# Kernel tuning notes

Hardware: AMD Instinct MI355X
Metric: run time of the kernel (lower is better)

Reference implementation:

```python
import jax, jax.numpy as jnp
import numpy as np

D_MODEL = 1024
NUM_HEADS = 16
D_K = D_MODEL // NUM_HEADS


def setup_inputs() -> dict:
    key = jax.random.key(0)
    ks = jax.random.split(key, 16)
    B, S, D = 4, 2048, D_MODEL
    scale = 1.0 / np.sqrt(D)
    inp = {
        'Xs': jax.random.normal(ks[0], (B, S, D), jnp.float32),
        'Xt': jax.random.normal(ks[1], (B, S, D), jnp.float32),
    }
    names = ['qs', 'qt', 'ks', 'kt', 'vs', 'vt']
    for i, n in enumerate(names):
        inp['W_' + n] = jax.random.normal(ks[2 + 2 * i], (D, D), jnp.float32) * scale
        inp['b_' + n] = jax.random.normal(ks[3 + 2 * i], (D,), jnp.float32) * 0.01
    inp['attn_bias'] = jnp.zeros((1, 1, 1, 1), jnp.float32)
    return inp


def _split_heads(x):
    B, S, _ = x.shape
    return x.reshape(B, S, NUM_HEADS, D_K).transpose(0, 2, 1, 3)  # (B,H,S,dk)


def reference(Xs, Xt, W_qs, b_qs, W_qt, b_qt, W_ks, b_ks, W_kt, b_kt,
              W_vs, b_vs, W_vt, b_vt, attn_bias):
    # Dual-linear fused projections: Linear(x) = x @ W.T + b (torch convention)
    Q = Xs @ W_qs.T + b_qs + Xt @ W_qt.T + b_qt
    K = Xs @ W_ks.T + b_ks + Xt @ W_kt.T + b_kt
    V = Xs @ W_vs.T + b_vs + Xt @ W_vt.T + b_vt
    Q, K, V = _split_heads(Q), _split_heads(K), _split_heads(V)
    scores = jnp.einsum('bhqd,bhkd->bhqk', Q, K) / jnp.sqrt(jnp.float32(D_K))
    scores = scores + attn_bias  # scalar learned bias, broadcast
    probs = jax.nn.softmax(scores, axis=-1)
    out = jnp.einsum('bhqk,bhkd->bhqd', probs, V)  # (B,H,S,dk)
    B, H, S, dk = out.shape
    return out.transpose(0, 2, 1, 3).reshape(B, S, H * dk)
```

## Files before the change

### kernel.cpp

```cpp
#include <hip/hip_runtime.h>
#include <hip/hip_bf16.h>

typedef __bf16 bf16;
typedef __attribute__((ext_vector_type(8))) __bf16 bf16x8;
typedef __attribute__((ext_vector_type(4))) __bf16 bf16x4;
typedef __attribute__((ext_vector_type(4))) float f32x4;

#define D_MODEL 1024
#define NHEAD 16
#define DK 64
#define BB 4
#define SS 2048
#define MM 8192
#define KK 2048
#define NN 3072

#define LDP 72
#define QSCALE 0.18033688011112042f

__device__ __forceinline__ void glds16(const bf16* g, bf16* s) {
    __builtin_amdgcn_global_load_lds(
        (const __attribute__((address_space(1))) void*)g,
        (__attribute__((address_space(3))) void*)s, 16, 0, 0);
}

__device__ __forceinline__ void pack_chunk(const float* __restrict__ src,
                                           bf16* __restrict__ dst,
                                           int row_off, int col_off, int idx) {
    int m = idx >> 7;
    int cl = idx & 127;
    const float4* s4 = (const float4*)&src[((size_t)m << 10) + cl * 8];
    float4 v0 = s4[0], v1 = s4[1];
    bf16x8 o;
    o[0]=(bf16)v0.x; o[1]=(bf16)v0.y; o[2]=(bf16)v0.z; o[3]=(bf16)v0.w;
    o[4]=(bf16)v1.x; o[5]=(bf16)v1.y; o[6]=(bf16)v1.z; o[7]=(bf16)v1.w;
    int r = row_off + m;
    int k = col_off + cl * 8;
    int mi = r & 127, mt = r >> 7;
    int c = (k >> 3) & 7, kt = k >> 6;
    int slot = mi * 8 + (c ^ (mi & 7));
    *(bf16x8*)&dst[(((((size_t)mt * 32 + kt) << 10) + slot) << 3)] = o;
}

__global__ void pack_all(const float* __restrict__ Xs, const float* __restrict__ Xt,
                         const float* __restrict__ Wqs, const float* __restrict__ Wqt,
                         const float* __restrict__ Wks, const float* __restrict__ Wkt,
                         const float* __restrict__ Wvs, const float* __restrict__ Wvt,
                         const float* __restrict__ bqs, const float* __restrict__ bqt,
                         const float* __restrict__ bks, const float* __restrict__ bkt,
                         const float* __restrict__ bvs, const float* __restrict__ bvt,
                         bf16* __restrict__ Xp, bf16* __restrict__ Wp,
                         float* __restrict__ biasc) {
    int blk = blockIdx.x;
    if (blk < 8192) {
        int i = blk * 256 + threadIdx.x;
        int sel = i >> 20;
        int idx = i & 1048575;
        pack_chunk(sel ? Xt : Xs, Xp, 0, sel ? 1024 : 0, idx);
        return;
    }
    if (blk < 11264) {
        int i = (blk - 8192) * 256 + threadIdx.x;
        int gi = i >> 17;
        int idx = i & 131071;
        const float* src = (gi == 0) ? Wqs : (gi == 1) ? Wqt : (gi == 2) ? Wks
                         : (gi == 3) ? Wkt : (gi == 4) ? Wvs : Wvt;
        pack_chunk(src, Wp, (gi >> 1) * 1024, (gi & 1) * 1024, idx);
        return;
    }
    for (int n = threadIdx.x; n < NN; n += 256) {
        int g = n >> 10, c = n & 1023;
        const float* a = (g == 0) ? bqs : ((g == 1) ? bks : bvs);
        const float* b = (g == 0) ? bqt : ((g == 1) ? bkt : bvt);
        biasc[n] = a[c] + b[c];
    }
}

#define VM8 asm volatile("s_waitcnt vmcnt(8)" ::: "memory")
#define VM0 asm volatile("s_waitcnt vmcnt(0)" ::: "memory")
#define VMNONE
#define LGKM0 asm volatile("s_waitcnt lgkmcnt(0)" ::: "memory")

#define STG(gsrc, ldst) do {                                                  \
    glds16((gsrc) + ((size_t)t << 3), (ldst) + (w << 9));                     \
    glds16((gsrc) + (((size_t)t + 512) << 3), (ldst) + ((w + 8) << 9));       \
  } while (0)

#define KSTEP(P, KT, DO_STAGE, VMOP) do {                                     \
    const bf16* aP = &sA[P][aH][0];                                           \
    const bf16* bP = &sB[P][bH][bR << 6];                                     \
    bf16x8 aF0[4][2], aF1[4][2], bF0[2][2], bF1[2][2];                        \
                                                       \
    _Pragma("unroll")                                                         \
    for (int mi = 0; mi < 4; mi++) {                                          \
      aF0[mi][0] = *(const bf16x8*)&aP[((mi*16+l16)<<6) + ((quad^swz)<<3)];   \
      aF0[mi][1] = *(const bf16x8*)&aP[((mi*16+l16)<<6) + (((4+quad)^swz)<<3)];\
    }                                                                         \
    _Pragma("unroll")                                                         \
    for (int ni = 0; ni < 2; ni++) {                                          \
      bF0[ni][0] = *(const bf16x8*)&bP[((ni*16+l16)<<6) + ((quad^swz)<<3)];   \
      bF0[ni][1] = *(const bf16x8*)&bP[((ni*16+l16)<<6) + (((4+quad)^swz)<<3)];\
    }                                                                         \
    __builtin_amdgcn_s_barrier(); LGKM0;                                      \
    __builtin_amdgcn_s_setprio(1);                                            \
    _Pragma("unroll")                                                         \
    for (int mi = 0; mi < 4; mi++)                                            \
      _Pragma("unroll")                                                       \
      for (int ni = 0; ni < 2; ni++) {                                        \
        acc[mi][ni] = __builtin_amdgcn_mfma_f32_16x16x32_bf16(aF0[mi][0], bF0[ni][0], acc[mi][ni], 0,0,0); \
        acc[mi][ni] = __builtin_amdgcn_mfma_f32_16x16x32_bf16(aF0[mi][1], bF0[ni][1], acc[mi][ni], 0,0,0); \
      }                                                                       \
    __builtin_amdgcn_s_setprio(0);                                            \
    __builtin_amdgcn_s_barrier();                                             \
                                                       \
    _Pragma("unroll")                                                         \
    for (int ni = 0; ni < 2; ni++) {                                          \
      bF1[ni][0] = *(const bf16x8*)&bP[(((ni+2)*16+l16)<<6) + ((quad^swz)<<3)]; \
      bF1[ni][1] = *(const bf16x8*)&bP[(((ni+2)*16+l16)<<6) + (((4+quad)^swz)<<3)]; \
    }                                                                         \
    __builtin_amdgcn_s_barrier(); LGKM0;                                      \
    __builtin_amdgcn_s_setprio(1);                                            \
    _Pragma("unroll")                                                         \
    for (int mi = 0; mi < 4; mi++)                                            \
      _Pragma("unroll")                                                       \
      for (int ni = 0; ni < 2; ni++) {                                        \
        acc[mi][ni+2] = __builtin_amdgcn_mfma_f32_16x16x32_bf16(aF0[mi][0], bF1[ni][0], acc[mi][ni+2], 0,0,0); \
        acc[mi][ni+2] = __builtin_amdgcn_mfma_f32_16x16x32_bf16(aF0[mi][1], bF1[ni][1], acc[mi][ni+2], 0,0,0); \
      }                                                                       \
    __builtin_amdgcn_s_setprio(0);                                            \
    __builtin_amdgcn_s_barrier();                                             \
                                       \
    _Pragma("unroll")                                                         \
    for (int mi = 0; mi < 4; mi++) {                                          \
      aF1[mi][0] = *(const bf16x8*)&aP[(((mi+4)*16+l16)<<6) + ((quad^swz)<<3)]; \
      aF1[mi][1] = *(const bf16x8*)&aP[(((mi+4)*16+l16)<<6) + (((4+quad)^swz)<<3)]; \
    }                                                                         \
    if (DO_STAGE) {                                                           \
      STG(Bg0 + ((size_t)((KT) + 2) << 13), &sB[P][0][0]);                    \
      STG(Bg1 + ((size_t)((KT) + 2) << 13), &sB[P][1][0]);                    \
    }                                                                         \
    __builtin_amdgcn_s_barrier(); LGKM0;                                      \
    __builtin_amdgcn_s_setprio(1);                                            \
    _Pragma("unroll")                                                         \
    for (int mi = 0; mi < 4; mi++)                                            \
      _Pragma("unroll")                                                       \
      for (int ni = 0; ni < 2; ni++) {                                        \
        acc[mi+4][ni+2] = __builtin_amdgcn_mfma_f32_16x16x32_bf16(aF1[mi][0], bF1[ni][0], acc[mi+4][ni+2], 0,0,0); \
        acc[mi+4][ni+2] = __builtin_amdgcn_mfma_f32_16x16x32_bf16(aF1[mi][1], bF1[ni][1], acc[mi+4][ni+2], 0,0,0); \
      }                                                                       \
    __builtin_amdgcn_s_setprio(0);                                            \
    __builtin_amdgcn_s_barrier();                                             \
                        \
    if (DO_STAGE) {                                                           \
      STG(Ag0 + ((size_t)((KT) + 2) << 13), &sA[P][0][0]);                    \
      STG(Ag1 + ((size_t)((KT) + 2) << 13), &sA[P][1][0]);                    \
    }                                                                         \
    __builtin_amdgcn_s_barrier();                                             \
    __builtin_amdgcn_s_setprio(1);                                            \
    _Pragma("unroll")                                                         \
    for (int mi = 0; mi < 4; mi++)                                            \
      _Pragma("unroll")                                                       \
      for (int ni = 0; ni < 2; ni++) {                                        \
        acc[mi+4][ni] = __builtin_amdgcn_mfma_f32_16x16x32_bf16(aF1[mi][0], bF0[ni][0], acc[mi+4][ni], 0,0,0); \
        acc[mi+4][ni] = __builtin_amdgcn_mfma_f32_16x16x32_bf16(aF1[mi][1], bF0[ni][1], acc[mi+4][ni], 0,0,0); \
      }                                                                       \
    __builtin_amdgcn_s_setprio(0);                                            \
    VMOP;                                                                     \
    __builtin_amdgcn_s_barrier();                                             \
    __builtin_amdgcn_sched_barrier(0);                                        \
  } while (0)

__global__ __launch_bounds__(512, 2) void gemm_qkv(
    const bf16* __restrict__ Xp, const bf16* __restrict__ Wp,
    const float* __restrict__ biasc,
    bf16* __restrict__ Qb, bf16* __restrict__ Kb, bf16* __restrict__ Vt) {
    __shared__ __align__(16) bf16 sA[2][2][8192];
    __shared__ __align__(16) bf16 sB[2][2][8192];

    const int t = threadIdx.x, lane = t & 63, w = t >> 6;
    const int quad = lane >> 4, l16 = lane & 15, swz = l16 & 7;
    const int wq = w & 3;
    const int wm = (w >> 2) * 128;
    const int wn = wq * 64;
    const int aH = w >> 2;
    const int bH = wq >> 1;
    const int bR = (wq & 1) * 64;

    const int bx = blockIdx.x, by = blockIdx.y;
    const bf16* Ag0 = Xp + (((size_t)(bx * 2 + 0) * 32) << 13);
    const bf16* Ag1 = Xp + (((size_t)(bx * 2 + 1) * 32) << 13);
    const bf16* Bg0 = Wp + (((size_t)(by * 2 + 0) * 32) << 13);
    const bf16* Bg1 = Wp + (((size_t)(by * 2 + 1) * 32) << 13);

    f32x4 acc[8][4] = {};

    STG(Ag0, &sA[0][0][0]); STG(Ag1, &sA[0][1][0]);
    STG(Bg0, &sB[0][0][0]); STG(Bg1, &sB[0][1][0]);
    STG(Ag0 + 8192, &sA[1][0][0]); STG(Ag1 + 8192, &sA[1][1][0]);
    STG(Bg0 + 8192, &sB[1][0][0]); STG(Bg1 + 8192, &sB[1][1][0]);
    VM8;
    __builtin_amdgcn_s_barrier();
    __builtin_amdgcn_sched_barrier(0);

    int kt = 0;
#pragma unroll 1
    for (int i = 0; i < 15; i++, kt += 2) {
        KSTEP(0, kt, 1, VM8);
        KSTEP(1, kt + 1, 1, VM8);
    }
    KSTEP(0, 30, 0, VM0);
    KSTEP(1, 31, 0, VMNONE);

    const int g = by >> 2;
    const int m00 = bx << 8, n00 = by << 8;
#pragma unroll
    for (int mi = 0; mi < 8; mi++) {
        int mbase = m00 + wm + mi * 16 + quad * 4;
#pragma unroll
        for (int ni = 0; ni < 4; ni++) {
            int n = n00 + wn + ni * 16 + l16;
            float bias = biasc[n];
            int c = n & 1023, h = c >> 6, d = c & 63;
#pragma unroll
            for (int r = 0; r < 4; r++) {
                int m = mbase + r;
                int b = m >> 11, s = m & 2047;
                size_t bh = (size_t)(b * NHEAD + h);
                float v = acc[mi][ni][r] + bias;
                if (g == 0)
                    Qb[(bh * SS + s) * DK + d] = (bf16)(v * QSCALE);
                else if (g == 1)
                    Kb[(bh * SS + s) * DK + d] = (bf16)v;
                else
                    Vt[(bh * DK + d) * SS + s] = (bf16)v;
            }
        }
    }
}

__global__ __launch_bounds__(256) void attn(
    const bf16* __restrict__ Qb, const bf16* __restrict__ Kb,
    const bf16* __restrict__ Vt, float* __restrict__ out) {
    __shared__ __align__(16) bf16 sK[64 * 64];
    __shared__ __align__(16) bf16 sV[64 * 64];
    __shared__ __align__(16) bf16 sP[4][32 * LDP];

    const int lid = blockIdx.x + gridDim.x * blockIdx.y;
    const int bh = (lid & 7) * 8 + ((lid >> 3) & 7);
    const int q0 = (lid >> 6) * 128;

    const int t = threadIdx.x;
    const int lane = t & 63, w = t >> 6;
    const int quad = lane >> 4, l16 = lane & 15, swz = l16 & 7;
    const int b = bh >> 4, h = bh & 15;

    const bf16* Qp = Qb + ((size_t)bh * SS + q0 + w * 32) * DK;
    bf16x8 qf[2][2];
#pragma unroll
    for (int f = 0; f < 2; f++)
#pragma unroll
        for (int kb = 0; kb < 2; kb++)
            qf[f][kb] = *(const bf16x8*)&Qp[(f * 16 + l16) * DK + kb * 32 + quad * 8];

    f32x4 o[2][4] = {};
    float lsum[2] = {0.f, 0.f};

    const bf16* Kp = Kb + (size_t)bh * SS * DK;
    const bf16* Vp = Vt + (size_t)bh * DK * SS;

    for (int kt = 0; kt < SS; kt += 64) {
#pragma unroll
        for (int j = 0; j < 2; j++) {
            int u = (w * 2 + j) * 64 + lane;
            int row = u >> 3;
            int cc = (u & 7) ^ (row & 7);
            glds16(Kp + (size_t)(kt + row) * DK + cc * 8, &sK[(w * 2 + j) * 512]);
            glds16(Vp + (size_t)row * SS + kt + cc * 8, &sV[(w * 2 + j) * 512]);
        }
        __syncthreads();

        f32x4 st[2][4] = {};
#pragma unroll
        for (int kb = 0; kb < 2; kb++)
#pragma unroll
            for (int ki = 0; ki < 4; ki++) {
                bf16x8 kf = *(const bf16x8*)&sK[(ki * 16 + l16) * 64 + (((kb * 4 + quad) ^ swz) * 8)];
                st[0][ki] = __builtin_amdgcn_mfma_f32_16x16x32_bf16(kf, qf[0][kb], st[0][ki], 0, 0, 0);
                st[1][ki] = __builtin_amdgcn_mfma_f32_16x16x32_bf16(kf, qf[1][kb], st[1][ki], 0, 0, 0);
            }

#pragma unroll
        for (int f = 0; f < 2; f++) {
            float ls = 0.f;
#pragma unroll
            for (int ki = 0; ki < 4; ki++) {
                float p0 = __builtin_amdgcn_exp2f(st[f][ki][0]);
                float p1 = __builtin_amdgcn_exp2f(st[f][ki][1]);
                float p2 = __builtin_amdgcn_exp2f(st[f][ki][2]);
                float p3 = __builtin_amdgcn_exp2f(st[f][ki][3]);
                ls += (p0 + p1) + (p2 + p3);
                bf16x4 pk;
                pk[0] = (bf16)p0; pk[1] = (bf16)p1; pk[2] = (bf16)p2; pk[3] = (bf16)p3;
                *(bf16x4*)&sP[w][(f * 16 + l16) * LDP + ki * 16 + quad * 4] = pk;
            }
            lsum[f] += ls;
        }

#pragma unroll
        for (int kb = 0; kb < 2; kb++) {
            bf16x8 af0 = *(const bf16x8*)&sP[w][(l16) * LDP + kb * 32 + quad * 8];
            bf16x8 af1 = *(const bf16x8*)&sP[w][(16 + l16) * LDP + kb * 32 + quad * 8];
#pragma unroll
            for (int ni = 0; ni < 4; ni++) {
                bf16x8 vf = *(const bf16x8*)&sV[(ni * 16 + l16) * 64 + (((kb * 4 + quad) ^ swz) * 8)];
                o[0][ni] = __builtin_amdgcn_mfma_f32_16x16x32_bf16(af0, vf, o[0][ni], 0, 0, 0);
                o[1][ni] = __builtin_amdgcn_mfma_f32_16x16x32_bf16(af1, vf, o[1][ni], 0, 0, 0);
            }
        }
        __syncthreads();
    }

#pragma unroll
    for (int f = 0; f < 2; f++) {
        lsum[f] += __shfl_xor(lsum[f], 16);
        lsum[f] += __shfl_xor(lsum[f], 32);
    }

    float* op = out + ((size_t)(b * SS + q0 + w * 32)) * D_MODEL + h * DK;
#pragma unroll
    for (int f = 0; f < 2; f++)
#pragma unroll
        for (int r = 0; r < 4; r++) {
            float linv = 1.0f / __shfl(lsum[f], quad * 4 + r);
#pragma unroll
            for (int ni = 0; ni < 4; ni++)
                op[(f * 16 + quad * 4 + r) * D_MODEL + ni * 16 + l16] = o[f][ni][r] * linv;
        }
}

extern "C" void kernel_launch(void* const* d_in, const int* in_sizes, int n_in,
                              void* d_out, int out_size, void* d_ws, size_t ws_size,
                              hipStream_t stream) {
    const float* Xs   = (const float*)d_in[0];
    const float* Xt   = (const float*)d_in[1];
    const float* Wqs  = (const float*)d_in[2];
    const float* bqs  = (const float*)d_in[3];
    const float* Wqt  = (const float*)d_in[4];
    const float* bqt  = (const float*)d_in[5];
    const float* Wks  = (const float*)d_in[6];
    const float* bks  = (const float*)d_in[7];
    const float* Wkt  = (const float*)d_in[8];
    const float* bkt  = (const float*)d_in[9];
    const float* Wvs  = (const float*)d_in[10];
    const float* bvs  = (const float*)d_in[11];
    const float* Wvt  = (const float*)d_in[12];
    const float* bvt  = (const float*)d_in[13];
    float* out = (float*)d_out;

    char* ws = (char*)d_ws;
    bf16*  Xp    = (bf16*)(ws);
    bf16*  Wp    = (bf16*)(ws + 33554432);
    float* biasc = (float*)(ws + 46137344);
    bf16*  Qb    = (bf16*)(ws + 46149632);
    bf16*  Kb    = (bf16*)(ws + 62926848);
    bf16*  Vt    = (bf16*)(ws + 79704064);

    pack_all<<<11265, 256, 0, stream>>>(Xs, Xt, Wqs, Wqt, Wks, Wkt, Wvs, Wvt,
                                        bqs, bqt, bks, bkt, bvs, bvt,
                                        Xp, Wp, biasc);

    gemm_qkv<<<dim3(MM / 256, NN / 256), 512, 0, stream>>>(Xp, Wp, biasc, Qb, Kb, Vt);

    attn<<<dim3(SS / 128, BB * NHEAD), 256, 0, stream>>>(Qb, Kb, Vt, out);
}
```

Before: 386.3 us.

## Shrink QKV GEMM M-tile to 128 and simplify the per-k-step MFMA schedule

The QKV projection GEMM block tile shrinks from 256x256 to 128x256. Each wave now owns a 64x64 output instead of 128x64, so there are fewer accumulators and one A stage per k-tile, and the grid doubles to 64x12 blocks. The four-phase k-step with many barriers becomes a two-phase step: load all fragments, run one half of the MFMAs, barrier, issue the global prefetch, then run the other half. This cuts barriers, register pressure and LDS use and may raise occupancy, at the cost of more loads of the weight operand per output and a lower MFMA-to-load ratio.

```diff
diff --git a/kernel.cpp b/kernel.cpp
--- a/kernel.cpp
+++ b/kernel.cpp
@@ -76,7 +76,7 @@
     }
 }
 
-#define VM8 asm volatile("s_waitcnt vmcnt(8)" ::: "memory")
+#define VM6 asm volatile("s_waitcnt vmcnt(6)" ::: "memory")
 #define VM0 asm volatile("s_waitcnt vmcnt(0)" ::: "memory")
 #define VMNONE
 #define LGKM0 asm volatile("s_waitcnt lgkmcnt(0)" ::: "memory")
@@ -86,84 +86,46 @@
     glds16((gsrc) + (((size_t)t + 512) << 3), (ldst) + ((w + 8) << 9));       \
   } while (0)
 
-#define KSTEP(P, KT, DO_STAGE, VMOP) do {                                     \
-    const bf16* aP = &sA[P][aH][0];                                           \
+#define TILE(P, KT, DO_STAGE, VMOP) do {                                      \
+    const bf16* aP = &sA[P][wm << 6];                                         \
     const bf16* bP = &sB[P][bH][bR << 6];                                     \
-    bf16x8 aF0[4][2], aF1[4][2], bF0[2][2], bF1[2][2];                        \
-                                                       \
-    _Pragma("unroll")                                                         \
-    for (int mi = 0; mi < 4; mi++) {                                          \
-      aF0[mi][0] = *(const bf16x8*)&aP[((mi*16+l16)<<6) + ((quad^swz)<<3)];   \
-      aF0[mi][1] = *(const bf16x8*)&aP[((mi*16+l16)<<6) + (((4+quad)^swz)<<3)];\
-    }                                                                         \
-    _Pragma("unroll")                                                         \
-    for (int ni = 0; ni < 2; ni++) {                                          \
-      bF0[ni][0] = *(const bf16x8*)&bP[((ni*16+l16)<<6) + ((quad^swz)<<3)];   \
-      bF0[ni][1] = *(const bf16x8*)&bP[((ni*16+l16)<<6) + (((4+quad)^swz)<<3)];\
-    }                                                                         \
-    __builtin_amdgcn_s_barrier(); LGKM0;                                      \
+    bf16x8 aF[4][2], bF[4][2];                                                \
+    _Pragma("unroll")                                                         \
+    for (int mi = 0; mi < 4; mi++)                                            \
+      aF[mi][0] = *(const bf16x8*)&aP[((mi*16+l16)<<6) + ((quad^swz)<<3)];    \
+    _Pragma("unroll")                                                         \
+    for (int ni = 0; ni < 4; ni++)                                            \
+      bF[ni][0] = *(const bf16x8*)&bP[((ni*16+l16)<<6) + ((quad^swz)<<3)];    \
+    _Pragma("unroll")                                                         \
+    for (int mi = 0; mi < 4; mi++)                                            \
+      aF[mi][1] = *(const bf16x8*)&aP[((mi*16+l16)<<6) + (((4+quad)^swz)<<3)];\
+    _Pragma("unroll")                                                         \
+    for (int ni = 0; ni < 4; ni++)                                            \
+      bF[ni][1] = *(const bf16x8*)&bP[((ni*16+l16)<<6) + (((4+quad)^swz)<<3)];\
     __builtin_amdgcn_s_setprio(1);                                            \
     _Pragma("unroll")                                                         \
     for (int mi = 0; mi < 4; mi++)                                            \
       _Pragma("unroll")                                                       \
-      for (int ni = 0; ni < 2; ni++) {                                        \
-        acc[mi][ni] = __builtin_amdgcn_mfma_f32_16x16x32_bf16(aF0[mi][0], bF0[ni][0], acc[mi][ni], 0,0,0); \
-        acc[mi][ni] = __builtin_amdgcn_mfma_f32_16x16x32_bf16(aF0[mi][1], bF0[ni][1], acc[mi][ni], 0,0,0); \
-      }                                                                       \
+      for (int ni = 0; ni < 4; ni++)                                          \
+        acc[mi][ni] = __builtin_amdgcn_mfma_f32_16x16x32_bf16(                \
+            aF[mi][0], bF[ni][0], acc[mi][ni], 0, 0, 0);                      \
     __builtin_amdgcn_s_setprio(0);                                            \
+    LGKM0;                                                                    \
+    __builtin_amdgcn_sched_barrier(0);                                        \
     __builtin_amdgcn_s_barrier();                                             \
-                                                       \
-    _Pragma("unroll")                                                         \
-    for (int ni = 0; ni < 2; ni++) {                                          \
-      bF1[ni][0] = *(const bf16x8*)&bP[(((ni+2)*16+l16)<<6) + ((quad^swz)<<3)]; \
-      bF1[ni][1] = *(const bf16x8*)&bP[(((ni+2)*16+l16)<<6) + (((4+quad)^swz)<<3)]; \
-    }                                                                         \
-    __builtin_amdgcn_s_barrier(); LGKM0;                                      \
-    __builtin_amdgcn_s_setprio(1);                                            \
-    _Pragma("unroll")                                                         \
-    for (int mi = 0; mi < 4; mi++)                                            \
-      _Pragma("unroll")                                                       \
-      for (int ni = 0; ni < 2; ni++) {                                        \
-        acc[mi][ni+2] = __builtin_amdgcn_mfma_f32_16x16x32_bf16(aF0[mi][0], bF1[ni][0], acc[mi][ni+2], 0,0,0); \
-        acc[mi][ni+2] = __builtin_amdgcn_mfma_f32_16x16x32_bf16(aF0[mi][1], bF1[ni][1], acc[mi][ni+2], 0,0,0); \
-      }                                                                       \
-    __builtin_amdgcn_s_setprio(0);                                            \
-    __builtin_amdgcn_s_barrier();                                             \
-                                       \
-    _Pragma("unroll")                                                         \
-    for (int mi = 0; mi < 4; mi++) {                                          \
-      aF1[mi][0] = *(const bf16x8*)&aP[(((mi+4)*16+l16)<<6) + ((quad^swz)<<3)]; \
-      aF1[mi][1] = *(const bf16x8*)&aP[(((mi+4)*16+l16)<<6) + (((4+quad)^swz)<<3)]; \
-    }                                                                         \
+    __builtin_amdgcn_sched_barrier(0);                                        \
     if (DO_STAGE) {                                                           \
+      STG(Ag  + ((size_t)((KT) + 2) << 13), &sA[P][0]);                       \
       STG(Bg0 + ((size_t)((KT) + 2) << 13), &sB[P][0][0]);                    \
       STG(Bg1 + ((size_t)((KT) + 2) << 13), &sB[P][1][0]);                    \
     }                                                                         \
-    __builtin_amdgcn_s_barrier(); LGKM0;                                      \
     __builtin_amdgcn_s_setprio(1);                                            \
     _Pragma("unroll")                                                         \
     for (int mi = 0; mi < 4; mi++)                                            \
       _Pragma("unroll")                                                       \
-      for (int ni = 0; ni < 2; ni++) {                                        \
-        acc[mi+4][ni+2] = __builtin_amdgcn_mfma_f32_16x16x32_bf16(aF1[mi][0], bF1[ni][0], acc[mi+4][ni+2], 0,0,0); \
-        acc[mi+4][ni+2] = __builtin_amdgcn_mfma_f32_16x16x32_bf16(aF1[mi][1], bF1[ni][1], acc[mi+4][ni+2], 0,0,0); \
-      }                                                                       \
-    __builtin_amdgcn_s_setprio(0);                                            \
-    __builtin_amdgcn_s_barrier();                                             \
-                        \
-    if (DO_STAGE) {                                                           \
-      STG(Ag0 + ((size_t)((KT) + 2) << 13), &sA[P][0][0]);                    \
-      STG(Ag1 + ((size_t)((KT) + 2) << 13), &sA[P][1][0]);                    \
-    }                                                                         \
-    __builtin_amdgcn_s_barrier();                                             \
-    __builtin_amdgcn_s_setprio(1);                                            \
-    _Pragma("unroll")                                                         \
-    for (int mi = 0; mi < 4; mi++)                                            \
-      _Pragma("unroll")                                                       \
-      for (int ni = 0; ni < 2; ni++) {                                        \
-        acc[mi+4][ni] = __builtin_amdgcn_mfma_f32_16x16x32_bf16(aF1[mi][0], bF0[ni][0], acc[mi+4][ni], 0,0,0); \
-        acc[mi+4][ni] = __builtin_amdgcn_mfma_f32_16x16x32_bf16(aF1[mi][1], bF0[ni][1], acc[mi+4][ni], 0,0,0); \
-      }                                                                       \
+      for (int ni = 0; ni < 4; ni++)                                          \
+        acc[mi][ni] = __builtin_amdgcn_mfma_f32_16x16x32_bf16(                \
+            aF[mi][1], bF[ni][1], acc[mi][ni], 0, 0, 0);                      \
     __builtin_amdgcn_s_setprio(0);                                            \
     VMOP;                                                                     \
     __builtin_amdgcn_s_barrier();                                             \
@@ -174,47 +136,43 @@
     const bf16* __restrict__ Xp, const bf16* __restrict__ Wp,
     const float* __restrict__ biasc,
     bf16* __restrict__ Qb, bf16* __restrict__ Kb, bf16* __restrict__ Vt) {
-    __shared__ __align__(16) bf16 sA[2][2][8192];
+    __shared__ __align__(16) bf16 sA[2][8192];
     __shared__ __align__(16) bf16 sB[2][2][8192];
 
     const int t = threadIdx.x, lane = t & 63, w = t >> 6;
     const int quad = lane >> 4, l16 = lane & 15, swz = l16 & 7;
     const int wq = w & 3;
-    const int wm = (w >> 2) * 128;
+    const int wm = (w >> 2) * 64;
     const int wn = wq * 64;
-    const int aH = w >> 2;
     const int bH = wq >> 1;
     const int bR = (wq & 1) * 64;
 
     const int bx = blockIdx.x, by = blockIdx.y;
-    const bf16* Ag0 = Xp + (((size_t)(bx * 2 + 0) * 32) << 13);
-    const bf16* Ag1 = Xp + (((size_t)(bx * 2 + 1) * 32) << 13);
+    const bf16* Ag  = Xp + (((size_t)bx * 32) << 13);
     const bf16* Bg0 = Wp + (((size_t)(by * 2 + 0) * 32) << 13);
     const bf16* Bg1 = Wp + (((size_t)(by * 2 + 1) * 32) << 13);
 
-    f32x4 acc[8][4] = {};
-
-    STG(Ag0, &sA[0][0][0]); STG(Ag1, &sA[0][1][0]);
-    STG(Bg0, &sB[0][0][0]); STG(Bg1, &sB[0][1][0]);
-    STG(Ag0 + 8192, &sA[1][0][0]); STG(Ag1 + 8192, &sA[1][1][0]);
-    STG(Bg0 + 8192, &sB[1][0][0]); STG(Bg1 + 8192, &sB[1][1][0]);
-    VM8;
+    f32x4 acc[4][4] = {};
+
+    STG(Ag, &sA[0][0]); STG(Bg0, &sB[0][0][0]); STG(Bg1, &sB[0][1][0]);
+    STG(Ag + 8192, &sA[1][0]); STG(Bg0 + 8192, &sB[1][0][0]); STG(Bg1 + 8192, &sB[1][1][0]);
+    VM6;
     __builtin_amdgcn_s_barrier();
     __builtin_amdgcn_sched_barrier(0);
 
     int kt = 0;
 #pragma unroll 1
     for (int i = 0; i < 15; i++, kt += 2) {
-        KSTEP(0, kt, 1, VM8);
-        KSTEP(1, kt + 1, 1, VM8);
-    }
-    KSTEP(0, 30, 0, VM0);
-    KSTEP(1, 31, 0, VMNONE);
+        TILE(0, kt, 1, VM6);
+        TILE(1, kt + 1, 1, VM6);
+    }
+    TILE(0, 30, 0, VM0);
+    TILE(1, 31, 0, VMNONE);
 
     const int g = by >> 2;
-    const int m00 = bx << 8, n00 = by << 8;
-#pragma unroll
-    for (int mi = 0; mi < 8; mi++) {
+    const int m00 = bx << 7, n00 = by << 8;
+#pragma unroll
+    for (int mi = 0; mi < 4; mi++) {
         int mbase = m00 + wm + mi * 16 + quad * 4;
 #pragma unroll
         for (int ni = 0; ni < 4; ni++) {
@@ -369,7 +327,7 @@
                                         bqs, bqt, bks, bkt, bvs, bvt,
                                         Xp, Wp, biasc);
 
-    gemm_qkv<<<dim3(MM / 256, NN / 256), 512, 0, stream>>>(Xp, Wp, biasc, Qb, Kb, Vt);
+    gemm_qkv<<<dim3(MM / 128, NN / 256), 512, 0, stream>>>(Xp, Wp, biasc, Qb, Kb, Vt);
 
     attn<<<dim3(SS / 128, BB * NHEAD), 256, 0, stream>>>(Qb, Kb, Vt, out);
 }
```

After: 370.5 us. 1.04x faster.
